# Kernel optimization log

Hardware: AMD Instinct MI355X
Metric: run time of the kernel (lower is better)

Reference implementation:

```python
import jax, jax.numpy as jnp
import numpy as np

TH_SIM_MIN = 0.9
TH_DIFF_MAX = 0.1
BIG = 1e9
EPS = 1e-8


def setup_inputs() -> dict:
    key = jax.random.key(0)
    k1, k2 = jax.random.split(key)
    B, T, D = 16, 2048, 128
    embeddings = jax.random.normal(k1, (B, T, D), dtype=jnp.float32)
    label = jax.random.randint(k2, (B, T), 0, 2, dtype=jnp.int32)
    return {"embeddings": embeddings, "label": label}


def _masked_mean(vals, row_mask):
    # mean of vals over rows where row_mask is True; 0-safe denominator
    cnt = jnp.sum(row_mask, axis=-1).astype(vals.dtype)
    s = jnp.sum(jnp.where(row_mask, vals, 0.0), axis=-1)
    return s / jnp.maximum(cnt, 1.0)


def reference(embeddings, label):
    B = embeddings.shape[0]
    # pairwise cosine similarity per batch: [B, T, T]
    w = jnp.linalg.norm(embeddings, axis=-1, keepdims=True)  # [B,T,1]
    sim = jnp.einsum('bid,bjd->bij', embeddings, embeddings)
    sim = sim / jnp.maximum(w * jnp.swapaxes(w, 1, 2), EPS)

    fake = (label == 0)  # [B,T]
    real = (label == 1)
    fake_col = fake[:, None, :]
    real_col = real[:, None, :]

    # f2f: for each fake i, min over fake j (diagonal included, as in torch)
    f2f_min = jnp.min(jnp.where(fake_col, sim, BIG), axis=2)
    loss_f2f = _masked_mean(jnp.maximum(TH_SIM_MIN - f2f_min, 0.0), fake)

    # r2r: for each real i, min over real j
    r2r_min = jnp.min(jnp.where(real_col, sim, BIG), axis=2)
    loss_r2r = _masked_mean(jnp.maximum(TH_SIM_MIN - r2r_min, 0.0), real)

    # f2r: for each fake i, max over real j
    f2r_max = jnp.max(jnp.where(real_col, sim, -BIG), axis=2)
    loss_f2r = _masked_mean(jnp.maximum(f2r_max - TH_DIFF_MAX, 0.0), fake)

    # r2f: for each real i, max over fake j
    r2f_max = jnp.max(jnp.where(fake_col, sim, -BIG), axis=2)
    loss_r2f = _masked_mean(jnp.maximum(r2f_max - TH_DIFF_MAX, 0.0), real)

    # torch code `continue`s (adds nothing) when either class is empty
    valid = (jnp.sum(fake, axis=1) > 0) & (jnp.sum(real, axis=1) > 0)
    per_batch = jnp.where(valid, loss_f2f + loss_r2r + loss_f2r + loss_r2f, 0.0)
    return jnp.sum(per_batch) / B
```

## Files before the change

kernel.cpp:

```cpp
#include <hip/hip_runtime.h>
#include <hip/hip_bf16.h>

typedef __bf16 bf16x8 __attribute__((ext_vector_type(8)));
typedef float  f32x4  __attribute__((ext_vector_type(4)));

namespace {
constexpr int kB = 16;
constexpr int kT = 2048;
constexpr int kD = 128;
constexpr int RB = 64;
constexpr int CT = 64;
constexpr float TH_SIM  = 0.9f;
constexpr float TH_DIFF = 0.1f;
constexpr float BIGF    = 1e9f;
}

static __device__ __forceinline__ void gload_lds16(const short* g, short* l) {
    __builtin_amdgcn_global_load_lds(
        (const __attribute__((address_space(1))) void*)g,
        (__attribute__((address_space(3))) void*)l, 16, 0, 0);
}

__global__ __launch_bounds__(256) void scan_kernel(const int* __restrict__ label,
                                                   int* __restrict__ perm,
                                                   int* __restrict__ cFarr) {
    const int b = blockIdx.x, tid = threadIdx.x;
    const int* lb = label + b * kT;
    int loc[8], cnt = 0;
    #pragma unroll
    for (int j = 0; j < 8; ++j) { loc[j] = (lb[tid * 8 + j] == 0); cnt += loc[j]; }
    __shared__ int s[256];
    s[tid] = cnt;
    __syncthreads();
    for (int off = 1; off < 256; off <<= 1) {
        const int v = (tid >= off) ? s[tid - off] : 0;
        __syncthreads();
        s[tid] += v;
        __syncthreads();
    }
    const int total = s[255];
    if (tid == 0) cFarr[b] = total;
    int run = s[tid] - cnt;
    #pragma unroll
    for (int j = 0; j < 8; ++j) {
        const int i = tid * 8 + j;
        perm[b * kT + i] = loc[j] ? run : (total + i - run);
        run += loc[j];
    }
}

__global__ __launch_bounds__(256) void nrm_kernel(const float* __restrict__ emb,
                                                  const int* __restrict__ perm,
                                                  __hip_bfloat16* __restrict__ out) {
    const int wave = threadIdx.x >> 6;
    const int lane = threadIdx.x & 63;
    const int row  = blockIdx.x * 4 + wave;
    const float2 v = *reinterpret_cast<const float2*>(emb + (size_t)row * kD + lane * 2);
    float ss = v.x * v.x + v.y * v.y;
    #pragma unroll
    for (int m = 1; m < 64; m <<= 1) ss += __shfl_xor(ss, m);
    const float inv = ss > 0.f ? rsqrtf(ss) : 0.f;
    const int b   = row >> 11;
    const int dst = perm[row];
    __hip_bfloat162 o;
    o.x = __float2bfloat16(v.x * inv);
    o.y = __float2bfloat16(v.y * inv);
    *reinterpret_cast<__hip_bfloat162*>(out + ((size_t)(b * kT + dst)) * kD + lane * 2) = o;
}

template <int MODE>
__device__ __forceinline__ void compute_tile(const short* __restrict__ buf,
                                             const bf16x8 (&afrag)[4],
                                             const float (&sgn)[4],
                                             float (&u1)[4], float (&u2)[4],
                                             int lo, int hi, int colBase, int cf) {
    #pragma unroll
    for (int g = 0; g < 4; ++g) {
        const int col = g * 16 + lo;
        bf16x8 bfrag[4];
        #pragma unroll
        for (int kk = 0; kk < 4; ++kk) {
            const int sh = (kk * 32 + hi * 8) ^ ((col & 7) << 3);
            bfrag[kk] = *reinterpret_cast<const bf16x8*>(&buf[col * kD + sh]);
        }
        f32x4 acc = {0.f, 0.f, 0.f, 0.f};
        #pragma unroll
        for (int kk = 0; kk < 4; ++kk)
            acc = __builtin_amdgcn_mfma_f32_16x16x32_bf16(afrag[kk], bfrag[kk], acc, 0, 0, 0);
        if (MODE == 0) {
            #pragma unroll
            for (int r = 0; r < 4; ++r) u1[r] = fminf(u1[r], acc[r] * sgn[r]);
        } else if (MODE == 1) {
            #pragma unroll
            for (int r = 0; r < 4; ++r) u2[r] = fminf(u2[r], -(acc[r] * sgn[r]));
        } else {
            const bool cfake = (colBase + col) < cf;
            #pragma unroll
            for (int r = 0; r < 4; ++r) {
                const float t = acc[r] * sgn[r];
                u1[r] = fminf(u1[r], cfake ? t : BIGF);
                u2[r] = fminf(u2[r], cfake ? BIGF : -t);
            }
        }
    }
}

__global__ __launch_bounds__(256, 2) void crloss_main(const __hip_bfloat16* __restrict__ nrm,
                                                      const int* __restrict__ cFarr,
                                                      float* __restrict__ partials) {
    __shared__ __align__(16) short lds[2][CT * kD];
    const int bid  = blockIdx.x;
    const int b    = bid >> 5;
    const int rb   = bid & 31;
    const int tid  = threadIdx.x;
    const int wave = tid >> 6;
    const int lane = tid & 63;
    const int lo   = lane & 15;
    const int hi   = lane >> 4;

    const short* nb = reinterpret_cast<const short*>(nrm) + (size_t)b * kT * kD;
    const int cf = cFarr[b];
    const int wave_row0 = rb * RB + wave * 16;

    bf16x8 afrag[4];
    #pragma unroll
    for (int kk = 0; kk < 4; ++kk)
        afrag[kk] = *reinterpret_cast<const bf16x8*>(
            nb + (size_t)(wave_row0 + lo) * kD + kk * 32 + hi * 8);

    float sgn[4];
    #pragma unroll
    for (int r = 0; r < 4; ++r)
        sgn[r] = (wave_row0 + hi * 4 + r < cf) ? 1.f : -1.f;

    float u1[4], u2[4];
    #pragma unroll
    for (int r = 0; r < 4; ++r) { u1[r] = BIGF; u2[r] = BIGF; }

    auto stage = [&](int ct, int bufIdx) {
        #pragma unroll
        for (int p = 0; p < 4; ++p) {
            const int unit = p * 4 + wave;
            const int c    = unit * 64 + lane;
            const int col  = c >> 4;
            const int sh   = ((c & 15) * 8) ^ ((col & 7) << 3);
            gload_lds16(nb + (size_t)(ct * CT + col) * kD + sh,
                        &lds[bufIdx][unit * 512]);
        }
    };

    const int  ctF    = cf >> 6;
    const bool hasMix = (cf & 63) != 0;

    stage(0, 0);
    __syncthreads();
    int cur = 0;
    for (int ct = 0; ct < kT / CT; ++ct) {
        if (ct + 1 < kT / CT) stage(ct + 1, cur ^ 1);
        if (ct < ctF)
            compute_tile<0>(lds[cur], afrag, sgn, u1, u2, lo, hi, ct * CT, cf);
        else if (ct == ctF && hasMix)
            compute_tile<2>(lds[cur], afrag, sgn, u1, u2, lo, hi, ct * CT, cf);
        else
            compute_tile<1>(lds[cur], afrag, sgn, u1, u2, lo, hi, ct * CT, cf);
        __syncthreads();
        cur ^= 1;
    }

    #pragma unroll
    for (int m = 1; m <= 8; m <<= 1) {
        #pragma unroll
        for (int r = 0; r < 4; ++r) {
            u1[r] = fminf(u1[r], __shfl_xor(u1[r], m));
            u2[r] = fminf(u2[r], __shfl_xor(u2[r], m));
        }
    }

    float sF = 0.f, sR = 0.f;
    if (lo == 0) {
        #pragma unroll
        for (int r = 0; r < 4; ++r) {
            const int  row = wave_row0 + hi * 4 + r;
            const bool f   = row < cf;
            const float mn = f ? u1[r] : u2[r];
            const float mx = f ? -u2[r] : -u1[r];
            const float l  = fmaxf(TH_SIM - mn, 0.f) + fmaxf(mx - TH_DIFF, 0.f);
            if (f) sF += l; else sR += l;
        }
    }
    #pragma unroll
    for (int m = 1; m < 64; m <<= 1) {
        sF += __shfl_xor(sF, m);
        sR += __shfl_xor(sR, m);
    }

    __shared__ float wsum[4][2];
    if (lane == 0) { wsum[wave][0] = sF; wsum[wave][1] = sR; }
    __syncthreads();
    if (tid == 0) {
        float a = 0.f, c = 0.f;
        for (int w = 0; w < 4; ++w) { a += wsum[w][0]; c += wsum[w][1]; }
        partials[bid * 2]     = a;
        partials[bid * 2 + 1] = c;
    }
}

__global__ __launch_bounds__(512) void crloss_final(const float* __restrict__ partials,
                                                    const int* __restrict__ cFarr,
                                                    float* __restrict__ out) {
    const int t = threadIdx.x;
    float pf = partials[t * 2];
    float pr = partials[t * 2 + 1];
    #pragma unroll
    for (int m = 1; m <= 16; m <<= 1) {
        pf += __shfl_xor(pf, m);
        pr += __shfl_xor(pr, m);
    }
    __shared__ float sF[16], sR[16];
    if ((t & 31) == 0) { sF[t >> 5] = pf; sR[t >> 5] = pr; }
    __syncthreads();
    if (t == 0) {
        float tot = 0.f;
        for (int b = 0; b < kB; ++b) {
            const int cf = cFarr[b], cr = kT - cf;
            if (cf > 0 && cr > 0)
                tot += sF[b] / (float)cf + sR[b] / (float)cr;
        }
        out[0] = tot / (float)kB;
    }
}

extern "C" void kernel_launch(void* const* d_in, const int* in_sizes, int n_in,
                              void* d_out, int out_size, void* d_ws, size_t ws_size,
                              hipStream_t stream) {
    const float* emb   = (const float*)d_in[0];
    const int*   label = (const int*)d_in[1];
    float*       out   = (float*)d_out;

    char* ws = (char*)d_ws;
    __hip_bfloat16* nrm = (__hip_bfloat16*)ws;
    int*   perm     = (int*)(ws + (size_t)kB * kT * kD * 2);
    int*   cFarr    = (int*)(ws + (size_t)kB * kT * kD * 2 + kB * kT * 4);
    float* partials = (float*)(ws + (size_t)kB * kT * kD * 2 + kB * kT * 4 + 64);

    scan_kernel<<<kB, 256, 0, stream>>>(label, perm, cFarr);
    nrm_kernel<<<kB * kT / 4, 256, 0, stream>>>(emb, perm, nrm);
    crloss_main<<<kB * (kT / RB), 256, 0, stream>>>(nrm, cFarr, partials);
    crloss_final<<<1, 512, 0, stream>>>(partials, cFarr, out);
}
```

Measured before the change: 50.86 us.

## Triple-buffer LDS tiles with vmcnt waits, fold sign into A, wave-level scan

The main kernel now keeps three LDS tile buffers in flight. It waits on explicit vmcnt counts and raw s_barrier instead of __syncthreads, so global-to-LDS loads overlap more with MFMA work, and it raises the occupancy hint to 3 blocks. The per-row sign multiply is removed by flipping the bf16 sign bits of the A fragment for real rows once up front, and MFMAs are wrapped in setprio. The label scan becomes one 1024-thread block that uses wave shuffles instead of an LDS scan with barriers. These changes trade higher LDS use per block and fragile hand-counted vmcnt values for fewer stalls.

```diff
diff --git a/kernel.cpp b/kernel.cpp
--- a/kernel.cpp
+++ b/kernel.cpp
@@ -10,9 +10,15 @@
 constexpr int kD = 128;
 constexpr int RB = 64;
 constexpr int CT = 64;
+constexpr int NT = kT / CT;
 constexpr float TH_SIM  = 0.9f;
 constexpr float TH_DIFF = 0.1f;
 constexpr float BIGF    = 1e9f;
+}
+
+template <int N>
+static __device__ __forceinline__ void wait_vmcnt() {
+    asm volatile("s_waitcnt vmcnt(%0)" :: "n"(N) : "memory");
 }
 
 static __device__ __forceinline__ void gload_lds16(const short* g, short* l) {
@@ -21,29 +27,28 @@
         (__attribute__((address_space(3))) void*)l, 16, 0, 0);
 }
 
-__global__ __launch_bounds__(256) void scan_kernel(const int* __restrict__ label,
-                                                   int* __restrict__ perm,
-                                                   int* __restrict__ cFarr) {
-    const int b = blockIdx.x, tid = threadIdx.x;
-    const int* lb = label + b * kT;
-    int loc[8], cnt = 0;
-    #pragma unroll
-    for (int j = 0; j < 8; ++j) { loc[j] = (lb[tid * 8 + j] == 0); cnt += loc[j]; }
-    __shared__ int s[256];
-    s[tid] = cnt;
-    __syncthreads();
-    for (int off = 1; off < 256; off <<= 1) {
-        const int v = (tid >= off) ? s[tid - off] : 0;
-        __syncthreads();
-        s[tid] += v;
-        __syncthreads();
-    }
-    const int total = s[255];
-    if (tid == 0) cFarr[b] = total;
-    int run = s[tid] - cnt;
-    #pragma unroll
-    for (int j = 0; j < 8; ++j) {
-        const int i = tid * 8 + j;
+__global__ __launch_bounds__(1024) void scan_kernel(const int* __restrict__ label,
+                                                    int* __restrict__ perm,
+                                                    int* __restrict__ cFarr) {
+    const int b    = threadIdx.x >> 6;
+    const int lane = threadIdx.x & 63;
+    const int* lb  = label + b * kT;
+    const int base = lane * 32;
+    int loc[32], cnt = 0;
+    #pragma unroll
+    for (int j = 0; j < 32; ++j) { loc[j] = (lb[base + j] == 0); cnt += loc[j]; }
+    int inc = cnt;
+    #pragma unroll
+    for (int m = 1; m < 64; m <<= 1) {
+        const int v = __shfl_up(inc, m);
+        if (lane >= m) inc += v;
+    }
+    const int total = __shfl(inc, 63);
+    if (lane == 0) cFarr[b] = total;
+    int run = inc - cnt;
+    #pragma unroll
+    for (int j = 0; j < 32; ++j) {
+        const int i = base + j;
         perm[b * kT + i] = loc[j] ? run : (total + i - run);
         run += loc[j];
     }
@@ -71,7 +76,6 @@
 template <int MODE>
 __device__ __forceinline__ void compute_tile(const short* __restrict__ buf,
                                              const bf16x8 (&afrag)[4],
-                                             const float (&sgn)[4],
                                              float (&u1)[4], float (&u2)[4],
                                              int lo, int hi, int colBase, int cf) {
     #pragma unroll
@@ -84,31 +88,32 @@
             bfrag[kk] = *reinterpret_cast<const bf16x8*>(&buf[col * kD + sh]);
         }
         f32x4 acc = {0.f, 0.f, 0.f, 0.f};
+        __builtin_amdgcn_s_setprio(1);
         #pragma unroll
         for (int kk = 0; kk < 4; ++kk)
             acc = __builtin_amdgcn_mfma_f32_16x16x32_bf16(afrag[kk], bfrag[kk], acc, 0, 0, 0);
+        __builtin_amdgcn_s_setprio(0);
         if (MODE == 0) {
             #pragma unroll
-            for (int r = 0; r < 4; ++r) u1[r] = fminf(u1[r], acc[r] * sgn[r]);
+            for (int r = 0; r < 4; ++r) u1[r] = fminf(u1[r], acc[r]);
         } else if (MODE == 1) {
             #pragma unroll
-            for (int r = 0; r < 4; ++r) u2[r] = fminf(u2[r], -(acc[r] * sgn[r]));
+            for (int r = 0; r < 4; ++r) u2[r] = fminf(u2[r], -acc[r]);
         } else {
             const bool cfake = (colBase + col) < cf;
             #pragma unroll
             for (int r = 0; r < 4; ++r) {
-                const float t = acc[r] * sgn[r];
-                u1[r] = fminf(u1[r], cfake ? t : BIGF);
-                u2[r] = fminf(u2[r], cfake ? BIGF : -t);
+                u1[r] = fminf(u1[r], cfake ? acc[r] : BIGF);
+                u2[r] = fminf(u2[r], cfake ? BIGF : -acc[r]);
             }
         }
     }
 }
 
-__global__ __launch_bounds__(256, 2) void crloss_main(const __hip_bfloat16* __restrict__ nrm,
+__global__ __launch_bounds__(256, 3) void crloss_main(const __hip_bfloat16* __restrict__ nrm,
                                                       const int* __restrict__ cFarr,
                                                       float* __restrict__ partials) {
-    __shared__ __align__(16) short lds[2][CT * kD];
+    __shared__ __align__(16) short lds[3][CT * kD];
     const int bid  = blockIdx.x;
     const int b    = bid >> 5;
     const int rb   = bid & 31;
@@ -128,10 +133,14 @@
         afrag[kk] = *reinterpret_cast<const bf16x8*>(
             nb + (size_t)(wave_row0 + lo) * kD + kk * 32 + hi * 8);
 
-    float sgn[4];
-    #pragma unroll
-    for (int r = 0; r < 4; ++r)
-        sgn[r] = (wave_row0 + hi * 4 + r < cf) ? 1.f : -1.f;
+    if (wave_row0 + lo >= cf) {
+        #pragma unroll
+        for (int kk = 0; kk < 4; ++kk) {
+            unsigned* u = reinterpret_cast<unsigned*>(&afrag[kk]);
+            #pragma unroll
+            for (int q = 0; q < 4; ++q) u[q] ^= 0x80008000u;
+        }
+    }
 
     float u1[4], u2[4];
     #pragma unroll
@@ -152,19 +161,22 @@
     const int  ctF    = cf >> 6;
     const bool hasMix = (cf & 63) != 0;
 
-    stage(0, 0);
-    __syncthreads();
-    int cur = 0;
-    for (int ct = 0; ct < kT / CT; ++ct) {
-        if (ct + 1 < kT / CT) stage(ct + 1, cur ^ 1);
+    stage(0, 0); stage(1, 1); stage(2, 2);
+    for (int ct = 0; ct < NT; ++ct) {
+        if (ct < NT - 2)       wait_vmcnt<8>();
+        else if (ct == NT - 2) wait_vmcnt<4>();
+        else                   wait_vmcnt<0>();
+        __builtin_amdgcn_s_barrier();
+        __builtin_amdgcn_sched_barrier(0);
+        const short* buf = lds[ct % 3];
         if (ct < ctF)
-            compute_tile<0>(lds[cur], afrag, sgn, u1, u2, lo, hi, ct * CT, cf);
+            compute_tile<0>(buf, afrag, u1, u2, lo, hi, ct * CT, cf);
         else if (ct == ctF && hasMix)
-            compute_tile<2>(lds[cur], afrag, sgn, u1, u2, lo, hi, ct * CT, cf);
+            compute_tile<2>(buf, afrag, u1, u2, lo, hi, ct * CT, cf);
         else
-            compute_tile<1>(lds[cur], afrag, sgn, u1, u2, lo, hi, ct * CT, cf);
-        __syncthreads();
-        cur ^= 1;
+            compute_tile<1>(buf, afrag, u1, u2, lo, hi, ct * CT, cf);
+        __builtin_amdgcn_s_barrier();
+        if (ct + 3 < NT) stage(ct + 3, ct % 3);
     }
 
     #pragma unroll
@@ -243,7 +255,7 @@
     int*   cFarr    = (int*)(ws + (size_t)kB * kT * kD * 2 + kB * kT * 4);
     float* partials = (float*)(ws + (size_t)kB * kT * kD * 2 + kB * kT * 4 + 64);
 
-    scan_kernel<<<kB, 256, 0, stream>>>(label, perm, cFarr);
+    scan_kernel<<<1, 1024, 0, stream>>>(label, perm, cFarr);
     nrm_kernel<<<kB * kT / 4, 256, 0, stream>>>(emb, perm, nrm);
     crloss_main<<<kB * (kT / RB), 256, 0, stream>>>(nrm, cFarr, partials);
     crloss_final<<<1, 512, 0, stream>>>(partials, cFarr, out);
```

Result: slower. 62.30 us (+22.5%).
